# Kernel tuning notes

Hardware: AMD Instinct MI355X
Metric: run time of the kernel (lower is better)

Reference implementation:

```python
import jax, jax.numpy as jnp
import numpy as np

SCALES = [2 ** i for i in range(11)]  # scales=10 -> [1,2,4,...,1024]


def _linear_upsample(x, N):
    """torch F.interpolate(mode='linear', align_corners=False) along last axis.
    x: (B, C, pn) -> (B, C, N)."""
    pn = x.shape[-1]
    scale = pn / N
    coords = (jnp.arange(N, dtype=x.dtype) + 0.5) * scale - 0.5
    coords = jnp.clip(coords, 0.0, pn - 1)
    i0 = jnp.floor(coords).astype(jnp.int32)
    i1 = jnp.minimum(i0 + 1, pn - 1)
    w = (coords - i0.astype(x.dtype))
    return x[..., i0] * (1.0 - w) + x[..., i1] * w


def setup_inputs() -> dict:
    key = jax.random.key(0)
    k1, k2 = jax.random.split(key)
    B, N, C, K = 32, 1024, 512, 4096
    f_BNC = jax.random.normal(k1, (B, N, C), dtype=jnp.float32)
    # torch init: uniform(-1/K, 1/K)
    codebook = (jax.random.uniform(k2, (K, C), dtype=jnp.float32) * 2.0 - 1.0) / K
    return {"f_BNC": f_BNC, "codebook": codebook}


def reference(f_BNC, codebook):
    f_BCN = jnp.transpose(f_BNC, (0, 2, 1))  # (B, C, N)
    B, C, N = f_BCN.shape
    f_ng = jax.lax.stop_gradient(f_BCN)      # f_no_grad
    f_rest = f_ng
    f_hat = jnp.zeros_like(f_ng)
    Wd = jax.lax.stop_gradient(codebook)     # embedding.weight.data for distances
    w_sq = jnp.sum(Wd * Wd, axis=1)          # (K,)
    SN = len(SCALES)
    commit = jnp.zeros((), dtype=f_BCN.dtype)
    qlat = jnp.zeros((), dtype=f_BCN.dtype)
    for pn in SCALES:
        # area downsample: exact block mean since N % pn == 0
        r = f_rest.reshape(B, C, pn, N // pn).mean(axis=-1)        # (B, C, pn)
        z = jnp.transpose(r, (0, 2, 1)).reshape(B * pn, C)          # (B*pn, C)
        d = jnp.sum(z * z, axis=1, keepdims=True) + w_sq - 2.0 * (z @ Wd.T)  # (B*pn, K)
        p = jax.nn.softmax(d, axis=-1)
        h = (p @ codebook).reshape(B, pn, C)                        # soft codebook lookup
        h = jnp.transpose(h, (0, 2, 1))                             # (B, C, pn)
        h = _linear_upsample(h, N)                                  # (B, C, N)
        f_hat = f_hat + h
        f_rest = f_rest - h
        commit = commit + 0.25 * jnp.mean((jax.lax.stop_gradient(f_hat) - f_BCN) ** 2)
        qlat = qlat + jnp.mean((f_hat - f_ng) ** 2)
    commit = commit / SN
    qlat = qlat / SN
    # straight-through estimator
    f_hat_st = jax.lax.stop_gradient(f_hat) - f_ng + f_BCN
    return jnp.transpose(f_hat_st, (0, 2, 1)), commit, qlat
```

## Files before the change

### kernel.cpp

```cpp
#include <hip/hip_runtime.h>
#include <hip/hip_bf16.h>

constexpr int B = 32, N = 1024, C = 512, K = 4096, SN = 11;
constexpr long BCN = (long)B * N * C;
constexpr int TKC = 128;
constexpr int NCH = K / TKC;
constexpr float PSCALE = 256.f;
constexpr int SCONE = 0x7f7f7f7f;

typedef __attribute__((ext_vector_type(4))) float f32x4;
typedef __attribute__((ext_vector_type(16))) float f32x16;
typedef __attribute__((ext_vector_type(8))) int i32x8;
typedef unsigned int u32;
typedef unsigned long u64;

static __device__ __forceinline__ short f2bf(float x) {
  __hip_bfloat16 h = __float2bfloat16(x);
  short s;
  __builtin_memcpy(&s, &h, sizeof(s));
  return s;
}
static __device__ __forceinline__ float bf2f(short s) {
  u32 u = ((u32)(unsigned short)s) << 16;
  float f;
  __builtin_memcpy(&f, &u, 4);
  return f;
}
static __device__ __forceinline__ u32 pk4_fp8(float a, float b, float c, float d) {
  int r = __builtin_amdgcn_cvt_pk_fp8_f32(a, b, 0, false);
  r = __builtin_amdgcn_cvt_pk_fp8_f32(c, d, r, true);
  return (u32)r;
}
static __device__ __forceinline__ f32x16 zero16() {
  f32x16 z;
#pragma unroll
  for (int i = 0; i < 16; ++i) z[i] = 0.f;
  return z;
}

__global__ __launch_bounds__(256) void wsq_kernel(const float* __restrict__ W,
                                                  float* __restrict__ wsq) {
  __shared__ float red[256];
  int k = blockIdx.x;
  const float* row = W + (long)k * C;
  float s = 0.f;
  for (int c = threadIdx.x; c < C; c += 256) {
    float v = row[c];
    s += v * v;
  }
  red[threadIdx.x] = s;
  __syncthreads();
  for (int off = 128; off > 0; off >>= 1) {
    if (threadIdx.x < off) red[threadIdx.x] += red[threadIdx.x + off];
    __syncthreads();
  }
  if (threadIdx.x == 0) wsq[k] = red[0];
}

__global__ __launch_bounds__(256) void colsum_kernel(const float* __restrict__ W,
                                                     float* __restrict__ csum) {
  int ch = blockIdx.x;
  const float* base = W + (long)ch * TKC * C;
  float s0 = 0.f, s1 = 0.f;
  for (int k = 0; k < TKC; ++k) {
    s0 += base[(long)k * C + threadIdx.x];
    s1 += base[(long)k * C + threadIdx.x + 256];
  }
  csum[ch * C + threadIdx.x] = s0;
  csum[ch * C + threadIdx.x + 256] = s1;
}

__global__ __launch_bounds__(256) void prep_w(const float* __restrict__ W,
                                              unsigned char* __restrict__ WnA,
                                              unsigned char* __restrict__ WtB) {
  __shared__ __attribute__((aligned(16))) unsigned char tile[32 * 520];
  const int blk = blockIdx.x, tid = threadIdx.x;
  const float* src = W + (long)blk * 32 * C;
#pragma unroll
  for (int i = 0; i < 16; ++i) {
    int idx = tid + i * 256;
    float4 v = ((const float4*)src)[idx];
    int key = idx >> 7, c = (idx & 127) * 4;
    *(u32*)&tile[key * 520 + c] = pk4_fp8(v.x, v.y, v.z, v.w);
  }
  __syncthreads();
#pragma unroll
  for (int i = 0; i < 2; ++i) {
    int slot = tid + i * 256;
    int cc = slot >> 6, L = slot & 63;
    const unsigned char* sp = &tile[(L & 31) * 520 + cc * 64 + (L >> 5) * 32];
    u64* dst = (u64*)(WnA + ((long)(blk * 8 + cc) * 64 + L) * 32);
    dst[0] = *(const u64*)(sp);
    dst[1] = *(const u64*)(sp + 8);
    dst[2] = *(const u64*)(sp + 16);
    dst[3] = *(const u64*)(sp + 24);
  }
#pragma unroll
  for (int i = 0; i < 2; ++i) {
    int slot = tid + i * 256;
    int c2 = slot >> 5, rho = slot & 31;
    union { unsigned char v[32]; u64 q[4]; } t;
#pragma unroll
    for (int j = 0; j < 32; ++j) t.v[j] = tile[j * 520 + c2 * 32 + rho];
    u64* dst = (u64*)(WtB + ((long)((blk >> 1) * 16 + c2) * 64 + (blk & 1) * 32 + rho) * 32);
    dst[0] = t.q[0]; dst[1] = t.q[1]; dst[2] = t.q[2]; dst[3] = t.q[3];
  }
}

__global__ __launch_bounds__(256) void init_f(const float* __restrict__ f,
                                              short* __restrict__ fbf,
                                              float* __restrict__ zpart) {
  int b = blockIdx.x >> 5;
  int n0 = (blockIdx.x & 31) * 32 + (threadIdx.x >> 7) * 16;
  int c4 = threadIdx.x & 127;
  float ax = 0, ay = 0, az = 0, aw = 0;
  for (int j = 0; j < 16; ++j) {
    long e = ((long)b * N + n0 + j) * 128 + c4;
    float4 v = ((const float4*)f)[e];
    short4 o = {f2bf(v.x), f2bf(v.y), f2bf(v.z), f2bf(v.w)};
    ((short4*)fbf)[e] = o;
    ax += v.x; ay += v.y; az += v.z; aw += v.w;
  }
  float4 zp = {ax, ay, az, aw};
  ((float4*)zpart)[((long)b * 64 + (n0 >> 4)) * 128 + c4] = zp;
}

__global__ __launch_bounds__(256) void reduce_zpart(const float* __restrict__ zpart,
                                                    unsigned char* __restrict__ zq, int pn) {
  long idx = (long)blockIdx.x * 256 + threadIdx.x;
  long tot = (long)B * pn * 128;
  if (idx >= tot) return;
  int c4 = (int)(idx & 127);
  long row = idx >> 7;
  int b = (int)(row / pn), j = (int)(row % pn);
  int r = 64 / pn;
  float ax = 0, ay = 0, az = 0, aw = 0;
  for (int i = 0; i < r; ++i) {
    float4 v = ((const float4*)zpart)[((long)b * 64 + j * r + i) * 128 + c4];
    ax += v.x; ay += v.y; az += v.z; aw += v.w;
  }
  float inv = (float)pn / (float)N;
  *(u32*)&zq[row * C + c4 * 4] = pk4_fp8(ax * inv, ay * inv, az * inv, aw * inv);
}

__global__ __launch_bounds__(256, 2) void flash_mfma(
    const unsigned char* __restrict__ zq, const unsigned char* __restrict__ WnA,
    const unsigned char* __restrict__ WtB, const float* __restrict__ wsq,
    const float* __restrict__ csum, short* __restrict__ hb,
    float* __restrict__ lpart, int M, int KS) {
  __shared__ __attribute__((aligned(16))) unsigned char ZS[16 * 2048];
  __shared__ __attribute__((aligned(16))) unsigned char PS[2][4 * 2048];
  const int tid = threadIdx.x;
  const int w = tid >> 6, lane = tid & 63;
  const int rho = lane & 31, hi = lane >> 5;
  const long row0 = (long)blockIdx.x * 64;
  const int nc = NCH / KS, ch0 = blockIdx.y * nc;

#pragma unroll
  for (int i = 0; i < 4; ++i) {
    int u = i * 4 + w, zt = u >> 3, cc = u & 7;
    long row = row0 + zt * 32 + rho;
    u64 v0 = 0, v1 = 0, v2 = 0, v3 = 0;
    if (row < M) {
      const u64* sp = (const u64*)(zq + row * C + cc * 64 + hi * 32);
      v0 = sp[0]; v1 = sp[1]; v2 = sp[2]; v3 = sp[3];
    }
    u64* dp = (u64*)(ZS + u * 2048 + lane * 32);
    dp[0] = v0; dp[1] = v1; dp[2] = v2; dp[3] = v3;
  }
  f32x16 hacc[2][4];
#pragma unroll
  for (int zt = 0; zt < 2; ++zt)
#pragma unroll
    for (int ct = 0; ct < 4; ++ct) hacc[zt][ct] = zero16();
  float lreg[2] = {0.f, 0.f};
  float cs[4] = {0.f, 0.f, 0.f, 0.f};
  __syncthreads();

#pragma unroll 1
  for (int ci = 0; ci < nc; ++ci) {
    const int ch = ch0 + ci;
#pragma unroll
    for (int ct = 0; ct < 4; ++ct) cs[ct] += csum[ch * C + w * 128 + ct * 32 + rho];
    f32x16 s[2];
    s[0] = zero16();
    s[1] = zero16();
    const unsigned char* wa = WnA + ((long)(ch * 4 + w) * 8) * 2048 + lane * 32;
    const unsigned char* zb = ZS + lane * 32;
#pragma unroll
    for (int cc = 0; cc < 8; ++cc) {
      i32x8 a = *(const i32x8*)(wa + cc * 2048);
      i32x8 b0 = *(const i32x8*)(zb + cc * 2048);
      i32x8 b1 = *(const i32x8*)(zb + (8 + cc) * 2048);
      s[0] = __builtin_amdgcn_mfma_scale_f32_32x32x64_f8f6f4(a, b0, s[0], 0, 0, 0, SCONE, 0, SCONE);
      s[1] = __builtin_amdgcn_mfma_scale_f32_32x32x64_f8f6f4(a, b1, s[1], 0, 0, 0, SCONE, 0, SCONE);
    }
    const float* wsb = wsq + ch * TKC + w * 32 + hi * 4;
    float wv[16];
#pragma unroll
    for (int g = 0; g < 4; ++g) {
      float4 t = *(const float4*)(wsb + 8 * g);
      wv[4 * g + 0] = t.x; wv[4 * g + 1] = t.y; wv[4 * g + 2] = t.z; wv[4 * g + 3] = t.w;
    }
    unsigned char* Pb = PS[ci & 1] + (w >> 1) * 2048 + (w & 1) * 1024 + rho * 32 + hi * 4;
#pragma unroll
    for (int zt = 0; zt < 2; ++zt) {
      float sum = 0.f, pv[16];
#pragma unroll
      for (int r = 0; r < 16; ++r) {
        float e = __expf(wv[r] - 2.f * s[zt][r]);
        sum += e;
        pv[r] = PSCALE * e - PSCALE;
      }
      lreg[zt] += sum;
#pragma unroll
      for (int g = 0; g < 4; ++g)
        *(u32*)(Pb + zt * 4096 + 8 * g) =
            pk4_fp8(pv[4 * g], pv[4 * g + 1], pv[4 * g + 2], pv[4 * g + 3]);
    }
    __syncthreads();
    const unsigned char* Pr = PS[ci & 1] + lane * 32;
    i32x8 pa[2][2];
#pragma unroll
    for (int zt = 0; zt < 2; ++zt)
#pragma unroll
      for (int f = 0; f < 2; ++f) pa[zt][f] = *(const i32x8*)(Pr + (zt * 2 + f) * 2048);
    const unsigned char* wb = WtB + ((long)(ch * 2) * 16 + w * 4) * 2048 + lane * 32;
#pragma unroll
    for (int f = 0; f < 2; ++f)
#pragma unroll
      for (int ct = 0; ct < 4; ++ct) {
        i32x8 bw = *(const i32x8*)(wb + (f * 16 + ct) * 2048);
        hacc[0][ct] = __builtin_amdgcn_mfma_scale_f32_32x32x64_f8f6f4(pa[0][f], bw, hacc[0][ct], 0, 0, 0, SCONE, 0, SCONE);
        hacc[1][ct] = __builtin_amdgcn_mfma_scale_f32_32x32x64_f8f6f4(pa[1][f], bw, hacc[1][ct], 0, 0, 0, SCONE, 0, SCONE);
      }
  }
  __syncthreads();
  lreg[0] += __shfl_xor(lreg[0], 32);
  lreg[1] += __shfl_xor(lreg[1], 32);
  float* l4 = (float*)PS;
  if (hi == 0) {
    l4[rho * 4 + w] = lreg[0];
    l4[(32 + rho) * 4 + w] = lreg[1];
  }
  __syncthreads();
  constexpr float PINV = 1.f / PSCALE;
  if (KS == 1) {
#pragma unroll
    for (int zt = 0; zt < 2; ++zt)
#pragma unroll
      for (int r = 0; r < 16; ++r) {
        int rr = zt * 32 + (r & 3) + 8 * (r >> 2) + 4 * hi;
        long row = row0 + rr;
        if (row < M) {
          float4 lv = ((const float4*)l4)[rr];
          float inv = 1.f / (lv.x + lv.y + lv.z + lv.w);
#pragma unroll
          for (int ct = 0; ct < 4; ++ct)
            hb[row * C + w * 128 + ct * 32 + rho] =
                f2bf((cs[ct] + hacc[zt][ct][r] * PINV) * inv);
        }
      }
  } else {
    long base = (long)blockIdx.y * M * C;
#pragma unroll
    for (int zt = 0; zt < 2; ++zt)
#pragma unroll
      for (int r = 0; r < 16; ++r) {
        int rr = zt * 32 + (r & 3) + 8 * (r >> 2) + 4 * hi;
        long row = row0 + rr;
        if (row < M) {
#pragma unroll
          for (int ct = 0; ct < 4; ++ct)
            hb[base + row * C + w * 128 + ct * 32 + rho] =
                f2bf(cs[ct] + hacc[zt][ct][r] * PINV);
        }
      }
    if (w == 0) {
      long row = row0 + lane;
      if (row < M) {
        float4 lv = ((const float4*)l4)[lane];
        lpart[(long)blockIdx.y * M + row] = lv.x + lv.y + lv.z + lv.w;
      }
    }
  }
}

__global__ __launch_bounds__(256) void combine_kernel(short* __restrict__ hb,
                                                      const float* __restrict__ lpart,
                                                      int M, int KS) {
  long idx = (long)blockIdx.x * 256 + threadIdx.x;
  long tot = (long)M * 128;
  if (idx >= tot) return;
  int m = (int)(idx >> 7);
  float lsum = 0.f;
  for (int s = 0; s < KS; ++s) lsum += lpart[(long)s * M + m];
  float ax = 0, ay = 0, az = 0, aw = 0;
  for (int s = 0; s < KS; ++s) {
    short4 v = ((const short4*)hb)[(long)s * tot + idx];
    ax += bf2f(v.x); ay += bf2f(v.y); az += bf2f(v.z); aw += bf2f(v.w);
  }
  float inv = 1.f / lsum;
  short4 o = {f2bf(ax * inv), f2bf(ay * inv), f2bf(az * inv), f2bf(aw * inv)};
  ((short4*)hb)[idx] = o;
}

__global__ __launch_bounds__(256) void fused_up(
    const short* __restrict__ hb, const short* __restrict__ fbf,
    const short* fhin, short* fhout, float* __restrict__ outf,
    unsigned char* __restrict__ zq, float* __restrict__ zpart,
    double* __restrict__ accum, int pn, int pn_next, int first, int last) {
  const int b = blockIdx.x >> 5;
  const int n0 = (blockIdx.x & 31) * 32 + (threadIdx.x >> 7) * 16;
  const int c4 = threadIdx.x & 127;
  const float scale = (float)pn * (1.f / (float)N);
  const int bs_next = pn_next ? (N / pn_next) : 0;
  float zx = 0, zy = 0, zz = 0, zw = 0, part = 0.f;
  for (int j = 0; j < 16; ++j) {
    int n = n0 + j;
    long e = ((long)b * N + n) * 128 + c4;
    float coords = ((float)n + 0.5f) * scale - 0.5f;
    coords = fminf(fmaxf(coords, 0.f), (float)(pn - 1));
    int i0 = (int)coords;
    int i1 = min(i0 + 1, pn - 1);
    float wq = coords - (float)i0, ow = 1.f - wq;
    short4 h0 = ((const short4*)hb)[((long)b * pn + i0) * 128 + c4];
    short4 h1 = ((const short4*)hb)[((long)b * pn + i1) * 128 + c4];
    short4 fv = ((const short4*)fbf)[e];
    float fhx, fhy, fhz, fhw;
    if (first) {
      fhx = fhy = fhz = fhw = 0.f;
    } else {
      short4 p = ((const short4*)fhin)[e];
      fhx = bf2f(p.x); fhy = bf2f(p.y); fhz = bf2f(p.z); fhw = bf2f(p.w);
    }
    fhx += bf2f(h0.x) * ow + bf2f(h1.x) * wq;
    fhy += bf2f(h0.y) * ow + bf2f(h1.y) * wq;
    fhz += bf2f(h0.z) * ow + bf2f(h1.z) * wq;
    fhw += bf2f(h0.w) * ow + bf2f(h1.w) * wq;
    if (last) {
      float4 o = {fhx, fhy, fhz, fhw};
      ((float4*)outf)[e] = o;
    } else {
      short4 o = {f2bf(fhx), f2bf(fhy), f2bf(fhz), f2bf(fhw)};
      ((short4*)fhout)[e] = o;
    }
    float dx = fhx - bf2f(fv.x), dy = fhy - bf2f(fv.y);
    float dz = fhz - bf2f(fv.z), dw = fhw - bf2f(fv.w);
    part += dx * dx + dy * dy + dz * dz + dw * dw;
    zx -= dx; zy -= dy; zz -= dz; zw -= dw;
    if (pn_next >= 64) {
      if (((n + 1) & (bs_next - 1)) == 0) {
        float inv = 1.f / (float)bs_next;
        *(u32*)&zq[((long)b * pn_next + n / bs_next) * C + c4 * 4] =
            pk4_fp8(zx * inv, zy * inv, zz * inv, zw * inv);
        zx = zy = zz = zw = 0.f;
      }
    }
  }
  if (pn_next && pn_next < 64) {
    float4 zp = {zx, zy, zz, zw};
    ((float4*)zpart)[((long)b * 64 + (n0 >> 4)) * 128 + c4] = zp;
  }
  __shared__ float red[256];
  red[threadIdx.x] = part;
  __syncthreads();
  for (int off = 128; off > 0; off >>= 1) {
    if (threadIdx.x < off) red[threadIdx.x] += red[threadIdx.x + off];
    __syncthreads();
  }
  if (threadIdx.x == 0) atomicAdd(&accum[blockIdx.x & 255], (double)red[0]);
}

__global__ void finalize_kernel(const double* __restrict__ accum,
                                float* __restrict__ out_scalars) {
  if (threadIdx.x == 0 && blockIdx.x == 0) {
    double s = 0.0;
    for (int i = 0; i < 256; ++i) s += accum[i];
    double denom = (double)SN * (double)BCN;
    out_scalars[0] = (float)(0.25 * s / denom);
    out_scalars[1] = (float)(s / denom);
  }
}

extern "C" void kernel_launch(void* const* d_in, const int* in_sizes, int n_in,
                              void* d_out, int out_size, void* d_ws, size_t ws_size,
                              hipStream_t stream) {
  const float* f = (const float*)d_in[0];
  const float* W = (const float*)d_in[1];
  float* out = (float*)d_out;

  const long MBy = 1l << 20;
  char* ws = (char*)d_ws;
  short* hb = (short*)ws;
  short* fbf = (short*)(ws + 32 * MBy);
  short* fhbf = (short*)(ws + 64 * MBy);
  unsigned char* zq = (unsigned char*)(ws + 96 * MBy);
  unsigned char* WnA = (unsigned char*)(ws + 112 * MBy);
  unsigned char* WtB = (unsigned char*)(ws + 114 * MBy);
  float* zpart = (float*)(ws + 116 * MBy);
  float* wsqf = (float*)(ws + 120 * MBy);
  float* csum = (float*)(ws + 120 * MBy + (1l << 16));
  float* lpart = (float*)(ws + 120 * MBy + (1l << 17));
  double* accum = (double*)(ws + 121 * MBy);

  hipMemsetAsync(accum, 0, 256 * sizeof(double), stream);

  wsq_kernel<<<K, 256, 0, stream>>>(W, wsqf);
  colsum_kernel<<<NCH, 256, 0, stream>>>(W, csum);
  prep_w<<<K / 32, 256, 0, stream>>>(W, WnA, WtB);
  init_f<<<B * 32, 256, 0, stream>>>(f, fbf, zpart);
  reduce_zpart<<<(B * 128 + 255) / 256, 256, 0, stream>>>(zpart, zq, 1);

  for (int s = 0; s < SN; ++s) {
    int pn = 1 << s;
    int M = B * pn;
    int gx = (M + 63) / 64;
    int KS = 512 / gx;
    if (KS < 1) KS = 1;
    if (KS > 32) KS = 32;
    flash_mfma<<<dim3(gx, KS), 256, 0, stream>>>(zq, WnA, WtB, wsqf, csum, hb, lpart, M, KS);
    if (KS > 1)
      combine_kernel<<<(int)(((long)M * 128 + 255) / 256), 256, 0, stream>>>(hb, lpart, M, KS);
    int pn_next = (s < SN - 1) ? (pn << 1) : 0;
    fused_up<<<B * 32, 256, 0, stream>>>(hb, fbf, fhbf, fhbf, out, zq, zpart, accum,
                                         pn, pn_next, s == 0 ? 1 : 0, s == SN - 1 ? 1 : 0);
    if (pn_next && pn_next < 64)
      reduce_zpart<<<(int)(((long)B * pn_next * 128 + 255) / 256), 256, 0, stream>>>(zpart, zq, pn_next);
  }

  finalize_kernel<<<1, 64, 0, stream>>>(accum, out + BCN);
}
```

Measured before the change: 945.1 us.

## Enlarge flash_mfma tile to 128 rows with LDS-staged, prefetched codebook chunks

flash_mfma now runs 512 threads per block and covers 128 rows instead of 64. Each codebook chunk's distance operand (WnA) is staged in a 64KB LDS buffer and shared across the two row halves. The next chunk is prefetched into registers and written to LDS while the softmax probabilities are computed. This halves the global codebook reads per row and overlaps loading with compute, but uses about 144KB of LDS, which may limit occupancy to one block per CU and halves the split-K parallelism for small scales.

```diff
diff --git a/kernel.cpp b/kernel.cpp
--- a/kernel.cpp
+++ b/kernel.cpp
@@ -11,6 +11,7 @@
 typedef __attribute__((ext_vector_type(4))) float f32x4;
 typedef __attribute__((ext_vector_type(16))) float f32x16;
 typedef __attribute__((ext_vector_type(8))) int i32x8;
+typedef __attribute__((ext_vector_type(4))) int i32x4;
 typedef unsigned int u32;
 typedef unsigned long u64;
 
@@ -143,22 +144,25 @@
   *(u32*)&zq[row * C + c4 * 4] = pk4_fp8(ax * inv, ay * inv, az * inv, aw * inv);
 }
 
-__global__ __launch_bounds__(256, 2) void flash_mfma(
+__global__ __launch_bounds__(512, 2) void flash_mfma(
     const unsigned char* __restrict__ zq, const unsigned char* __restrict__ WnA,
     const unsigned char* __restrict__ WtB, const float* __restrict__ wsq,
     const float* __restrict__ csum, short* __restrict__ hb,
     float* __restrict__ lpart, int M, int KS) {
-  __shared__ __attribute__((aligned(16))) unsigned char ZS[16 * 2048];
-  __shared__ __attribute__((aligned(16))) unsigned char PS[2][4 * 2048];
+  __shared__ __attribute__((aligned(16))) unsigned char lds[147456];
+  unsigned char* ZS = lds;
+  unsigned char* WA = lds + 65536;
+  unsigned char* PS = lds + 131072;
   const int tid = threadIdx.x;
   const int w = tid >> 6, lane = tid & 63;
   const int rho = lane & 31, hi = lane >> 5;
-  const long row0 = (long)blockIdx.x * 64;
+  const int kg = w & 3, zp = w >> 2;
+  const long row0 = (long)blockIdx.x * 128;
   const int nc = NCH / KS, ch0 = blockIdx.y * nc;
 
 #pragma unroll
   for (int i = 0; i < 4; ++i) {
-    int u = i * 4 + w, zt = u >> 3, cc = u & 7;
+    int u = w * 4 + i, zt = u >> 3, cc = u & 7;
     long row = row0 + zt * 32 + rho;
     u64 v0 = 0, v1 = 0, v2 = 0, v3 = 0;
     if (row < M) {
@@ -168,118 +172,160 @@
     u64* dp = (u64*)(ZS + u * 2048 + lane * 32);
     dp[0] = v0; dp[1] = v1; dp[2] = v2; dp[3] = v3;
   }
-  f32x16 hacc[2][4];
-#pragma unroll
-  for (int zt = 0; zt < 2; ++zt)
-#pragma unroll
-    for (int ct = 0; ct < 4; ++ct) hacc[zt][ct] = zero16();
+  {
+    const i32x4* gsrc = (const i32x4*)(WnA + (long)ch0 * 65536);
+#pragma unroll
+    for (int i = 0; i < 8; ++i) {
+      i32x4 v = gsrc[tid + i * 512];
+      *(i32x4*)(WA + (tid + i * 512) * 16) = v;
+    }
+  }
+  f32x16 hacc[4][2];
+#pragma unroll
+  for (int zt = 0; zt < 4; ++zt) {
+    hacc[zt][0] = zero16();
+    hacc[zt][1] = zero16();
+  }
   float lreg[2] = {0.f, 0.f};
-  float cs[4] = {0.f, 0.f, 0.f, 0.f};
+  float cs[2] = {0.f, 0.f};
   __syncthreads();
 
 #pragma unroll 1
   for (int ci = 0; ci < nc; ++ci) {
     const int ch = ch0 + ci;
-#pragma unroll
-    for (int ct = 0; ct < 4; ++ct) cs[ct] += csum[ch * C + w * 128 + ct * 32 + rho];
-    f32x16 s[2];
-    s[0] = zero16();
-    s[1] = zero16();
-    const unsigned char* wa = WnA + ((long)(ch * 4 + w) * 8) * 2048 + lane * 32;
-    const unsigned char* zb = ZS + lane * 32;
+    cs[0] += csum[ch * C + (2 * w) * 32 + rho];
+    cs[1] += csum[ch * C + (2 * w + 1) * 32 + rho];
+    f32x16 s0 = zero16(), s1 = zero16();
+    const unsigned char* wa = WA + kg * 8 * 2048 + lane * 32;
+    const unsigned char* zb = ZS + zp * 16 * 2048 + lane * 32;
 #pragma unroll
     for (int cc = 0; cc < 8; ++cc) {
       i32x8 a = *(const i32x8*)(wa + cc * 2048);
       i32x8 b0 = *(const i32x8*)(zb + cc * 2048);
       i32x8 b1 = *(const i32x8*)(zb + (8 + cc) * 2048);
-      s[0] = __builtin_amdgcn_mfma_scale_f32_32x32x64_f8f6f4(a, b0, s[0], 0, 0, 0, SCONE, 0, SCONE);
-      s[1] = __builtin_amdgcn_mfma_scale_f32_32x32x64_f8f6f4(a, b1, s[1], 0, 0, 0, SCONE, 0, SCONE);
-    }
-    const float* wsb = wsq + ch * TKC + w * 32 + hi * 4;
+      s0 = __builtin_amdgcn_mfma_scale_f32_32x32x64_f8f6f4(a, b0, s0, 0, 0, 0, SCONE, 0, SCONE);
+      s1 = __builtin_amdgcn_mfma_scale_f32_32x32x64_f8f6f4(a, b1, s1, 0, 0, 0, SCONE, 0, SCONE);
+    }
+    const unsigned char* wb = WtB + ((long)(ch * 2) * 16 + 2 * w) * 2048 + lane * 32;
+    i32x8 wb00 = *(const i32x8*)(wb);
+    i32x8 wb01 = *(const i32x8*)(wb + 2048);
+    const bool have_next = (ci + 1 < nc);
+    i32x4 st[8];
+    if (have_next) {
+      const i32x4* gsrc = (const i32x4*)(WnA + (long)(ch + 1) * 65536);
+#pragma unroll
+      for (int i = 0; i < 8; ++i) st[i] = gsrc[tid + i * 512];
+    }
+    asm volatile("s_waitcnt lgkmcnt(0)" ::: "memory");
+    __builtin_amdgcn_s_barrier();
+    const float* wsb = wsq + ch * TKC + kg * 32 + hi * 4;
     float wv[16];
 #pragma unroll
     for (int g = 0; g < 4; ++g) {
       float4 t = *(const float4*)(wsb + 8 * g);
       wv[4 * g + 0] = t.x; wv[4 * g + 1] = t.y; wv[4 * g + 2] = t.z; wv[4 * g + 3] = t.w;
     }
-    unsigned char* Pb = PS[ci & 1] + (w >> 1) * 2048 + (w & 1) * 1024 + rho * 32 + hi * 4;
-#pragma unroll
-    for (int zt = 0; zt < 2; ++zt) {
+    const int pbase = (kg & 1) * 1024 + rho * 32 + hi * 4;
+    {
       float sum = 0.f, pv[16];
 #pragma unroll
       for (int r = 0; r < 16; ++r) {
-        float e = __expf(wv[r] - 2.f * s[zt][r]);
+        float e = __expf(wv[r] - 2.f * s0[r]);
         sum += e;
         pv[r] = PSCALE * e - PSCALE;
       }
-      lreg[zt] += sum;
+      lreg[0] += sum;
+      unsigned char* Pun = PS + ((2 * zp) * 2 + (kg >> 1)) * 2048;
 #pragma unroll
       for (int g = 0; g < 4; ++g)
-        *(u32*)(Pb + zt * 4096 + 8 * g) =
+        *(u32*)(Pun + pbase + 8 * g) =
             pk4_fp8(pv[4 * g], pv[4 * g + 1], pv[4 * g + 2], pv[4 * g + 3]);
     }
-    __syncthreads();
-    const unsigned char* Pr = PS[ci & 1] + lane * 32;
-    i32x8 pa[2][2];
-#pragma unroll
-    for (int zt = 0; zt < 2; ++zt)
-#pragma unroll
-      for (int f = 0; f < 2; ++f) pa[zt][f] = *(const i32x8*)(Pr + (zt * 2 + f) * 2048);
-    const unsigned char* wb = WtB + ((long)(ch * 2) * 16 + w * 4) * 2048 + lane * 32;
-#pragma unroll
-    for (int f = 0; f < 2; ++f)
-#pragma unroll
-      for (int ct = 0; ct < 4; ++ct) {
-        i32x8 bw = *(const i32x8*)(wb + (f * 16 + ct) * 2048);
-        hacc[0][ct] = __builtin_amdgcn_mfma_scale_f32_32x32x64_f8f6f4(pa[0][f], bw, hacc[0][ct], 0, 0, 0, SCONE, 0, SCONE);
-        hacc[1][ct] = __builtin_amdgcn_mfma_scale_f32_32x32x64_f8f6f4(pa[1][f], bw, hacc[1][ct], 0, 0, 0, SCONE, 0, SCONE);
-      }
+    if (have_next) {
+#pragma unroll
+      for (int i = 0; i < 8; ++i)
+        *(i32x4*)(WA + (tid + i * 512) * 16) = st[i];
+    }
+    {
+      float sum = 0.f, pv[16];
+#pragma unroll
+      for (int r = 0; r < 16; ++r) {
+        float e = __expf(wv[r] - 2.f * s1[r]);
+        sum += e;
+        pv[r] = PSCALE * e - PSCALE;
+      }
+      lreg[1] += sum;
+      unsigned char* Pun = PS + ((2 * zp + 1) * 2 + (kg >> 1)) * 2048;
+#pragma unroll
+      for (int g = 0; g < 4; ++g)
+        *(u32*)(Pun + pbase + 8 * g) =
+            pk4_fp8(pv[4 * g], pv[4 * g + 1], pv[4 * g + 2], pv[4 * g + 3]);
+    }
+    asm volatile("s_waitcnt lgkmcnt(0)" ::: "memory");
+    __builtin_amdgcn_s_barrier();
+    __builtin_amdgcn_sched_barrier(0);
+#pragma unroll
+    for (int f = 0; f < 2; ++f) {
+      const unsigned char* Pf = PS + f * 2048 + lane * 32;
+      i32x8 pa[4];
+#pragma unroll
+      for (int zt = 0; zt < 4; ++zt) pa[zt] = *(const i32x8*)(Pf + zt * 4096);
+      i32x8 bw0, bw1;
+      if (f == 0) {
+        bw0 = wb00;
+        bw1 = wb01;
+      } else {
+        bw0 = *(const i32x8*)(wb + 16 * 2048);
+        bw1 = *(const i32x8*)(wb + 17 * 2048);
+      }
+#pragma unroll
+      for (int zt = 0; zt < 4; ++zt) {
+        hacc[zt][0] = __builtin_amdgcn_mfma_scale_f32_32x32x64_f8f6f4(pa[zt], bw0, hacc[zt][0], 0, 0, 0, SCONE, 0, SCONE);
+        hacc[zt][1] = __builtin_amdgcn_mfma_scale_f32_32x32x64_f8f6f4(pa[zt], bw1, hacc[zt][1], 0, 0, 0, SCONE, 0, SCONE);
+      }
+    }
   }
   __syncthreads();
   lreg[0] += __shfl_xor(lreg[0], 32);
   lreg[1] += __shfl_xor(lreg[1], 32);
   float* l4 = (float*)PS;
   if (hi == 0) {
-    l4[rho * 4 + w] = lreg[0];
-    l4[(32 + rho) * 4 + w] = lreg[1];
+    l4[((2 * zp) * 32 + rho) * 4 + kg] = lreg[0];
+    l4[((2 * zp + 1) * 32 + rho) * 4 + kg] = lreg[1];
   }
   __syncthreads();
   constexpr float PINV = 1.f / PSCALE;
   if (KS == 1) {
 #pragma unroll
-    for (int zt = 0; zt < 2; ++zt)
+    for (int zt = 0; zt < 4; ++zt)
 #pragma unroll
       for (int r = 0; r < 16; ++r) {
-        int rr = zt * 32 + (r & 3) + 8 * (r >> 2) + 4 * hi;
-        long row = row0 + rr;
+        int rl = zt * 32 + (r & 3) + 8 * (r >> 2) + 4 * hi;
+        long row = row0 + rl;
         if (row < M) {
-          float4 lv = ((const float4*)l4)[rr];
+          float4 lv = ((const float4*)l4)[rl];
           float inv = 1.f / (lv.x + lv.y + lv.z + lv.w);
-#pragma unroll
-          for (int ct = 0; ct < 4; ++ct)
-            hb[row * C + w * 128 + ct * 32 + rho] =
-                f2bf((cs[ct] + hacc[zt][ct][r] * PINV) * inv);
+          hb[row * C + (2 * w) * 32 + rho] = f2bf((cs[0] + hacc[zt][0][r] * PINV) * inv);
+          hb[row * C + (2 * w + 1) * 32 + rho] = f2bf((cs[1] + hacc[zt][1][r] * PINV) * inv);
         }
       }
   } else {
     long base = (long)blockIdx.y * M * C;
 #pragma unroll
-    for (int zt = 0; zt < 2; ++zt)
+    for (int zt = 0; zt < 4; ++zt)
 #pragma unroll
       for (int r = 0; r < 16; ++r) {
-        int rr = zt * 32 + (r & 3) + 8 * (r >> 2) + 4 * hi;
-        long row = row0 + rr;
+        int rl = zt * 32 + (r & 3) + 8 * (r >> 2) + 4 * hi;
+        long row = row0 + rl;
         if (row < M) {
-#pragma unroll
-          for (int ct = 0; ct < 4; ++ct)
-            hb[base + row * C + w * 128 + ct * 32 + rho] =
-                f2bf(cs[ct] + hacc[zt][ct][r] * PINV);
+          hb[base + row * C + (2 * w) * 32 + rho] = f2bf(cs[0] + hacc[zt][0][r] * PINV);
+          hb[base + row * C + (2 * w + 1) * 32 + rho] = f2bf(cs[1] + hacc[zt][1][r] * PINV);
         }
       }
-    if (w == 0) {
-      long row = row0 + lane;
+    if (tid < 128) {
+      long row = row0 + tid;
       if (row < M) {
-        float4 lv = ((const float4*)l4)[lane];
+        float4 lv = ((const float4*)l4)[tid];
         lpart[(long)blockIdx.y * M + row] = lv.x + lv.y + lv.z + lv.w;
       }
     }
@@ -415,11 +461,11 @@
   for (int s = 0; s < SN; ++s) {
     int pn = 1 << s;
     int M = B * pn;
-    int gx = (M + 63) / 64;
-    int KS = 512 / gx;
+    int gx = (M + 127) / 128;
+    int KS = 256 / gx;
     if (KS < 1) KS = 1;
     if (KS > 32) KS = 32;
-    flash_mfma<<<dim3(gx, KS), 256, 0, stream>>>(zq, WnA, WtB, wsqf, csum, hb, lpart, M, KS);
+    flash_mfma<<<dim3(gx, KS), 512, 0, stream>>>(zq, WnA, WtB, wsqf, csum, hb, lpart, M, KS);
     if (KS > 1)
       combine_kernel<<<(int)(((long)M * 128 + 255) / 256), 256, 0, stream>>>(hb, lpart, M, KS);
     int pn_next = (s < SN - 1) ? (pn << 1) : 0;
```

New measurement: 2.486 ms. 163% more time.
